# Performance work log

Measured on AMD Instinct MI355X. Metric: run time of the kernel, lower is better.

Reference implementation:

```python
import jax, jax.numpy as jnp
import numpy as np

N, E, D = 100000, 1280000, 64


def setup_inputs() -> dict:
    key = jax.random.key(0)
    ks = jax.random.split(key, 9)
    x = jax.random.normal(ks[0], (N, D), jnp.float32)
    edge_index = jax.random.randint(ks[1], (2, E), 0, N, dtype=jnp.int64)
    edge_weight = jax.random.uniform(ks[2], (E,), jnp.float32)
    s = 1.0 / np.sqrt(D)
    W0 = jax.random.normal(ks[3], (D, D), jnp.float32) * s
    b0 = jnp.zeros((D,), jnp.float32)
    W1 = jax.random.normal(ks[4], (D, D), jnp.float32) * s
    b1 = jnp.zeros((D,), jnp.float32)
    W2 = jax.random.normal(ks[5], (D, D), jnp.float32) * s
    b2 = jnp.zeros((D,), jnp.float32)
    return {"x": x, "edge_index": edge_index, "edge_weight": edge_weight,
            "W0": W0, "b0": b0, "W1": W1, "b1": b1, "W2": W2, "b2": b2}


def reference(x, edge_index, edge_weight, W0, b0, W1, b1, W2, b2):
    n = x.shape[0]
    row, col = edge_index[0], edge_index[1]
    # GCN normalization with self-loops (PyG gcn_norm, fill_value=1)
    loop = jnp.arange(n)
    row_f = jnp.concatenate([row, loop])
    col_f = jnp.concatenate([col, loop])
    w_f = jnp.concatenate([edge_weight, jnp.ones((n,), x.dtype)])
    deg = jax.ops.segment_sum(w_f, col_f, num_segments=n)
    dinv = jnp.where(deg > 0, jax.lax.rsqrt(deg), 0.0).astype(x.dtype)
    norm = dinv[row_f] * w_f * dinv[col_f]  # [E+N]

    def conv(h, W, b):
        h = h @ W                                  # [N, D_out]
        msg = h[row_f] * norm[:, None]             # gather + scale
        return jax.ops.segment_sum(msg, col_f, num_segments=n) + b

    results = [x]
    h = jax.nn.relu(conv(x, W0, b0))   # dropout p=0 / eval -> identity
    results.append(h)
    h = jax.nn.relu(conv(h, W1, b1))
    results.append(h)
    h = conv(h, W2, b2)                # last layer: no activation
    results.append(h)
    return tuple(results)
```

## Files before the change

### kernel.cpp

```cpp
#include <hip/hip_runtime.h>
#include <hip/hip_fp16.h>


#define TPB 256
#define ECAP 64
#define LCAP 6

typedef _Float16 half8 __attribute__((ext_vector_type(8)));
typedef float f32x4 __attribute__((ext_vector_type(4)));

__global__ __launch_bounds__(TPB) void k_scatter(const int* __restrict__ row,
                                                 const int* __restrict__ col,
                                                 const float* __restrict__ w,
                                                 int* __restrict__ degcnt,
                                                 long long* __restrict__ edges, int E) {
    int i = blockIdx.x * TPB + threadIdx.x;
    if (i >= E) return;
    int c = col[i];
    int r = atomicAdd(&degcnt[c], 1);
    if (r < ECAP)
        edges[((size_t)c << LCAP) + r] =
            ((long long)(unsigned)__float_as_int(w[i]) << 32) | (unsigned)row[i];
}

__global__ __launch_bounds__(TPB) void k_dinv(const long long* __restrict__ edges,
                                              const int* __restrict__ degcnt,
                                              float* __restrict__ dinv, int n) {
    int node = blockIdx.x * (TPB / 64) + (threadIdx.x >> 6);
    if (node >= n) return;
    int lane = threadIdx.x & 63;
    int cnt = min(degcnt[node], ECAP);
    float wv = 0.f;
    if (lane < cnt)
        wv = __int_as_float((int)(edges[((size_t)node << LCAP) + lane] >> 32));
    #pragma unroll
    for (int off = 1; off < 64; off <<= 1) wv += __shfl_xor(wv, off);
    if (lane == 0) dinv[node] = rsqrtf(1.0f + wv);
}

__global__ __launch_bounds__(TPB, 4) void k_gemm64(const float* __restrict__ in,
                                                   const float* __restrict__ Wg,
                                                   __half* __restrict__ hwh,
                                                   const float* __restrict__ dinvg,
                                                   float* __restrict__ cp, int n) {
    __shared__ _Float16 As[128 * 64];
    __shared__ _Float16 Bs[64 * 64];
    int tid = threadIdx.x;
    int rowbase = blockIdx.x * 128;

    {
        const float4* W4 = (const float4*)Wg;
        #pragma unroll
        for (int it = 0; it < 4; ++it) {
            int k = (tid >> 4) + 16 * it;
            int n0 = (tid & 15) * 4;
            float4 wv = W4[k * 16 + (tid & 15)];
            #pragma unroll
            for (int j = 0; j < 4; ++j) {
                int nn = n0 + j;
                float e = (j == 0) ? wv.x : (j == 1) ? wv.y : (j == 2) ? wv.z : wv.w;
                Bs[nn * 64 + (((k >> 3) ^ (nn & 7)) << 3) + (k & 7)] = (_Float16)e;
            }
        }
    }
    {
        int r = tid >> 1;
        int gr = rowbase + r;
        int c0 = (tid & 1) * 32;
        float di = (gr < n) ? dinvg[gr] : 0.f;
        const float4* A4 = (const float4*)in;
        #pragma unroll
        for (int j = 0; j < 4; ++j) {
            float4 v0 = make_float4(0.f, 0.f, 0.f, 0.f);
            float4 v1 = v0;
            if (gr < n) {
                v0 = A4[(size_t)gr * 16 + (c0 >> 2) + j * 2];
                v1 = A4[(size_t)gr * 16 + (c0 >> 2) + j * 2 + 1];
                if (cp) {
                    *(float4*)&cp[((size_t)gr * 16 + (c0 >> 2) + j * 2) * 4] = v0;
                    *(float4*)&cp[((size_t)gr * 16 + (c0 >> 2) + j * 2 + 1) * 4] = v1;
                }
            }
            int c4 = (c0 >> 3) + j;
            half8 hv;
            hv[0] = (_Float16)(v0.x * di); hv[1] = (_Float16)(v0.y * di);
            hv[2] = (_Float16)(v0.z * di); hv[3] = (_Float16)(v0.w * di);
            hv[4] = (_Float16)(v1.x * di); hv[5] = (_Float16)(v1.y * di);
            hv[6] = (_Float16)(v1.z * di); hv[7] = (_Float16)(v1.w * di);
            *(half8*)&As[r * 64 + ((c4 ^ (r & 7)) << 3)] = hv;
        }
    }
    __syncthreads();

    int w = tid >> 6;
    int lane = tid & 63;
    int l15 = lane & 15, l4 = lane >> 4;
    f32x4 acc[2][4];
    #pragma unroll
    for (int mt = 0; mt < 2; ++mt)
        #pragma unroll
        for (int nt = 0; nt < 4; ++nt) acc[mt][nt] = (f32x4){0.f, 0.f, 0.f, 0.f};
    const half8* Av = (const half8*)As;
    const half8* Bv = (const half8*)Bs;
    #pragma unroll
    for (int kk = 0; kk < 2; ++kk) {
        int ck = kk * 4 + l4;
        half8 a0 = Av[(w * 32 + l15) * 8 + (ck ^ (l15 & 7))];
        half8 a1 = Av[(w * 32 + 16 + l15) * 8 + (ck ^ (l15 & 7))];
        #pragma unroll
        for (int nt = 0; nt < 4; ++nt) {
            half8 b = Bv[(nt * 16 + l15) * 8 + (ck ^ (l15 & 7))];
            acc[0][nt] = __builtin_amdgcn_mfma_f32_16x16x32_f16(a0, b, acc[0][nt], 0, 0, 0);
            acc[1][nt] = __builtin_amdgcn_mfma_f32_16x16x32_f16(a1, b, acc[1][nt], 0, 0, 0);
        }
    }
    __syncthreads();

    #pragma unroll
    for (int mt = 0; mt < 2; ++mt)
        #pragma unroll
        for (int nt = 0; nt < 4; ++nt)
            #pragma unroll
            for (int rg = 0; rg < 4; ++rg) {
                int r = w * 32 + mt * 16 + l4 * 4 + rg;
                int c = nt * 16 + l15;
                As[r * 64 + (((c >> 3) ^ (r & 7)) << 3) + (c & 7)] =
                    (_Float16)acc[mt][nt][rg];
            }
    __syncthreads();
    #pragma unroll
    for (int it = 0; it < 4; ++it) {
        int idx = it * 256 + tid;
        int r = idx >> 3, c4 = idx & 7;
        int gr = rowbase + r;
        if (gr < n) {
            half8 hv = *(const half8*)&As[r * 64 + ((c4 ^ (r & 7)) << 3)];
            *(half8*)&hwh[(size_t)gr * 64 + c4 * 8] = hv;
        }
    }
}

__global__ __launch_bounds__(TPB) void k_gather(const int* __restrict__ degcnt,
                                                const long long* __restrict__ epk,
                                                const __half* __restrict__ hwh,
                                                const float* __restrict__ dinv,
                                                const float* __restrict__ b,
                                                float* __restrict__ out,
                                                int n, int relu) {
    int node = __builtin_amdgcn_readfirstlane(blockIdx.x * (TPB / 64) + (threadIdx.x >> 6));
    if (node >= n) return;
    int lane = threadIdx.x & 63;
    int cnt = min(degcnt[node], ECAP);
    int s0 = node << LCAP;
    int s1 = s0 + cnt;
    float acc = 0.f;
    int e = s0;
    for (; e + 8 <= s1; e += 8) {
        long long v0 = epk[e + 0];
        long long v1 = epk[e + 1];
        long long v2 = epk[e + 2];
        long long v3 = epk[e + 3];
        long long v4 = epk[e + 4];
        long long v5 = epk[e + 5];
        long long v6 = epk[e + 6];
        long long v7 = epk[e + 7];
        float h0 = __half2float(hwh[(size_t)(int)v0 * 64 + lane]);
        float h1 = __half2float(hwh[(size_t)(int)v1 * 64 + lane]);
        float h2 = __half2float(hwh[(size_t)(int)v2 * 64 + lane]);
        float h3 = __half2float(hwh[(size_t)(int)v3 * 64 + lane]);
        float h4 = __half2float(hwh[(size_t)(int)v4 * 64 + lane]);
        float h5 = __half2float(hwh[(size_t)(int)v5 * 64 + lane]);
        float h6 = __half2float(hwh[(size_t)(int)v6 * 64 + lane]);
        float h7 = __half2float(hwh[(size_t)(int)v7 * 64 + lane]);
        acc = fmaf(h0, __int_as_float((int)(v0 >> 32)), acc);
        acc = fmaf(h1, __int_as_float((int)(v1 >> 32)), acc);
        acc = fmaf(h2, __int_as_float((int)(v2 >> 32)), acc);
        acc = fmaf(h3, __int_as_float((int)(v3 >> 32)), acc);
        acc = fmaf(h4, __int_as_float((int)(v4 >> 32)), acc);
        acc = fmaf(h5, __int_as_float((int)(v5 >> 32)), acc);
        acc = fmaf(h6, __int_as_float((int)(v6 >> 32)), acc);
        acc = fmaf(h7, __int_as_float((int)(v7 >> 32)), acc);
    }
    if (e + 4 <= s1) {
        long long v0 = epk[e + 0];
        long long v1 = epk[e + 1];
        long long v2 = epk[e + 2];
        long long v3 = epk[e + 3];
        float h0 = __half2float(hwh[(size_t)(int)v0 * 64 + lane]);
        float h1 = __half2float(hwh[(size_t)(int)v1 * 64 + lane]);
        float h2 = __half2float(hwh[(size_t)(int)v2 * 64 + lane]);
        float h3 = __half2float(hwh[(size_t)(int)v3 * 64 + lane]);
        acc = fmaf(h0, __int_as_float((int)(v0 >> 32)), acc);
        acc = fmaf(h1, __int_as_float((int)(v1 >> 32)), acc);
        acc = fmaf(h2, __int_as_float((int)(v2 >> 32)), acc);
        acc = fmaf(h3, __int_as_float((int)(v3 >> 32)), acc);
        e += 4;
    }
    if (e + 2 <= s1) {
        long long v0 = epk[e + 0];
        long long v1 = epk[e + 1];
        float h0 = __half2float(hwh[(size_t)(int)v0 * 64 + lane]);
        float h1 = __half2float(hwh[(size_t)(int)v1 * 64 + lane]);
        acc = fmaf(h0, __int_as_float((int)(v0 >> 32)), acc);
        acc = fmaf(h1, __int_as_float((int)(v1 >> 32)), acc);
        e += 2;
    }
    if (e < s1) {
        long long v0 = epk[e];
        float h0 = __half2float(hwh[(size_t)(int)v0 * 64 + lane]);
        acc = fmaf(h0, __int_as_float((int)(v0 >> 32)), acc);
    }
    float di = dinv[node];
    float self = __half2float(hwh[(size_t)node * 64 + lane]);
    float o = fmaf(self + acc, di, b[lane]);
    if (relu) o = o > 0.f ? o : 0.f;
    out[(size_t)node * 64 + lane] = o;
}

extern "C" void kernel_launch(void* const* d_in, const int* in_sizes, int n_in,
                              void* d_out, int out_size, void* d_ws, size_t ws_size,
                              hipStream_t stream) {
    const float* x = (const float*)d_in[0];
    const int* ei = (const int*)d_in[1];
    const float* ew = (const float*)d_in[2];
    const float* Wl[3] = {(const float*)d_in[3], (const float*)d_in[5], (const float*)d_in[7]};
    const float* Bl[3] = {(const float*)d_in[4], (const float*)d_in[6], (const float*)d_in[8]};

    const int n = in_sizes[0] / 64;
    const int E = in_sizes[2];
    const int* row = ei;
    const int* col = ei + E;
    float* out = (float*)d_out;

    char* ws = (char*)d_ws;
    size_t o = 0;
    float* dinv       = (float*)(ws + o);    o = (o + (size_t)n * 4 + 255) & ~(size_t)255;
    __half* hwh       = (__half*)(ws + o);   o = (o + (size_t)n * 128 + 255) & ~(size_t)255;
    int* degcnt       = (int*)(ws + o);      o = (o + (size_t)n * 4 + 255) & ~(size_t)255;
    long long* edges  = (long long*)(ws + o);

    hipMemsetAsync(degcnt, 0, (size_t)n * 4, stream);
    k_scatter<<<(E + TPB - 1) / TPB, TPB, 0, stream>>>(row, col, ew, degcnt, edges, E);
    k_dinv<<<(n * 64 + TPB - 1) / TPB, TPB, 0, stream>>>(edges, degcnt, dinv, n);

    const float* hin = x;
    for (int L = 0; L < 3; ++L) {
        float* oseg = out + (size_t)(L + 1) * n * 64;
        k_gemm64<<<(n + 127) / 128, TPB, 0, stream>>>(hin, Wl[L], hwh, dinv, L == 0 ? out : nullptr, n);
        k_gather<<<(n * 64 + TPB - 1) / TPB, TPB, 0, stream>>>(degcnt, edges, hwh, dinv, Bl[L], oseg, n, L < 2 ? 1 : 0);
        hin = oseg;
    }
}
```

Baseline: 402.3 us.

## Fuse degree weight sum into scatter and drop separate dinv kernel

The scatter kernel now accumulates the per-node edge-weight sum with a float atomicAdd into a 64-byte-strided metadata record next to the count, and each thread handles two edges. This removes the separate k_dinv kernel launch and its pass over the edge lists. The gemm and gather kernels recompute rsqrt(1+wsum) on the fly. In exchange the scatter does a second atomic per edge, the memset grows from n*4 to n*64 bytes, and reads of count and weight sum now stride 64 bytes per node.

Result: slower. 434.1 us (+7.9%).

```diff
diff --git a/kernel.cpp b/kernel.cpp
--- a/kernel.cpp
+++ b/kernel.cpp
@@ -12,41 +12,41 @@
 __global__ __launch_bounds__(TPB) void k_scatter(const int* __restrict__ row,
                                                  const int* __restrict__ col,
                                                  const float* __restrict__ w,
-                                                 int* __restrict__ degcnt,
-                                                 long long* __restrict__ edges, int E) {
-    int i = blockIdx.x * TPB + threadIdx.x;
-    if (i >= E) return;
-    int c = col[i];
-    int r = atomicAdd(&degcnt[c], 1);
-    if (r < ECAP)
-        edges[((size_t)c << LCAP) + r] =
-            ((long long)(unsigned)__float_as_int(w[i]) << 32) | (unsigned)row[i];
-}
-
-__global__ __launch_bounds__(TPB) void k_dinv(const long long* __restrict__ edges,
-                                              const int* __restrict__ degcnt,
-                                              float* __restrict__ dinv, int n) {
-    int node = blockIdx.x * (TPB / 64) + (threadIdx.x >> 6);
-    if (node >= n) return;
-    int lane = threadIdx.x & 63;
-    int cnt = min(degcnt[node], ECAP);
-    float wv = 0.f;
-    if (lane < cnt)
-        wv = __int_as_float((int)(edges[((size_t)node << LCAP) + lane] >> 32));
-    #pragma unroll
-    for (int off = 1; off < 64; off <<= 1) wv += __shfl_xor(wv, off);
-    if (lane == 0) dinv[node] = rsqrtf(1.0f + wv);
+                                                 int* __restrict__ meta,
+                                                 long long* __restrict__ edges,
+                                                 int E, int half) {
+    int t = blockIdx.x * TPB + threadIdx.x;
+    if (t < half) {
+        int c = col[t];
+        float wv = w[t];
+        int r = atomicAdd(&meta[(size_t)c << 4], 1);
+        atomicAdd((float*)(meta + ((size_t)c << 4) + 1), wv);
+        if (r < ECAP)
+            edges[((size_t)c << LCAP) + r] =
+                ((long long)(unsigned)__float_as_int(wv) << 32) | (unsigned)row[t];
+    }
+    int t2 = t + half;
+    if (t2 < E) {
+        int c = col[t2];
+        float wv = w[t2];
+        int r = atomicAdd(&meta[(size_t)c << 4], 1);
+        atomicAdd((float*)(meta + ((size_t)c << 4) + 1), wv);
+        if (r < ECAP)
+            edges[((size_t)c << LCAP) + r] =
+                ((long long)(unsigned)__float_as_int(wv) << 32) | (unsigned)row[t2];
+    }
 }
 
 __global__ __launch_bounds__(TPB, 4) void k_gemm64(const float* __restrict__ in,
                                                    const float* __restrict__ Wg,
                                                    __half* __restrict__ hwh,
-                                                   const float* __restrict__ dinvg,
+                                                   const int* __restrict__ meta,
                                                    float* __restrict__ cp, int n) {
     __shared__ _Float16 As[128 * 64];
     __shared__ _Float16 Bs[64 * 64];
     int tid = threadIdx.x;
     int rowbase = blockIdx.x * 128;
+    const float* metaF = (const float*)meta;
 
     {
         const float4* W4 = (const float4*)Wg;
@@ -67,7 +67,8 @@
         int r = tid >> 1;
         int gr = rowbase + r;
         int c0 = (tid & 1) * 32;
-        float di = (gr < n) ? dinvg[gr] : 0.f;
+        float di = 0.f;
+        if (gr < n) di = rsqrtf(1.0f + metaF[((size_t)gr << 4) + 1]);
         const float4* A4 = (const float4*)in;
         #pragma unroll
         for (int j = 0; j < 4; ++j) {
@@ -140,17 +141,17 @@
     }
 }
 
-__global__ __launch_bounds__(TPB) void k_gather(const int* __restrict__ degcnt,
+__global__ __launch_bounds__(TPB) void k_gather(const int* __restrict__ meta,
                                                 const long long* __restrict__ epk,
                                                 const __half* __restrict__ hwh,
-                                                const float* __restrict__ dinv,
                                                 const float* __restrict__ b,
                                                 float* __restrict__ out,
                                                 int n, int relu) {
     int node = __builtin_amdgcn_readfirstlane(blockIdx.x * (TPB / 64) + (threadIdx.x >> 6));
     if (node >= n) return;
     int lane = threadIdx.x & 63;
-    int cnt = min(degcnt[node], ECAP);
+    int cnt = min(meta[(size_t)node << 4], ECAP);
+    float wsum = ((const float*)meta)[((size_t)node << 4) + 1];
     int s0 = node << LCAP;
     int s1 = s0 + cnt;
     float acc = 0.f;
@@ -210,7 +211,7 @@
         float h0 = __half2float(hwh[(size_t)(int)v0 * 64 + lane]);
         acc = fmaf(h0, __int_as_float((int)(v0 >> 32)), acc);
     }
-    float di = dinv[node];
+    float di = rsqrtf(1.0f + wsum);
     float self = __half2float(hwh[(size_t)node * 64 + lane]);
     float o = fmaf(self + acc, di, b[lane]);
     if (relu) o = o > 0.f ? o : 0.f;
@@ -234,20 +235,19 @@
 
     char* ws = (char*)d_ws;
     size_t o = 0;
-    float* dinv       = (float*)(ws + o);    o = (o + (size_t)n * 4 + 255) & ~(size_t)255;
     __half* hwh       = (__half*)(ws + o);   o = (o + (size_t)n * 128 + 255) & ~(size_t)255;
-    int* degcnt       = (int*)(ws + o);      o = (o + (size_t)n * 4 + 255) & ~(size_t)255;
+    int* meta         = (int*)(ws + o);      o = (o + (size_t)n * 64 + 255) & ~(size_t)255;
     long long* edges  = (long long*)(ws + o);
 
-    hipMemsetAsync(degcnt, 0, (size_t)n * 4, stream);
-    k_scatter<<<(E + TPB - 1) / TPB, TPB, 0, stream>>>(row, col, ew, degcnt, edges, E);
-    k_dinv<<<(n * 64 + TPB - 1) / TPB, TPB, 0, stream>>>(edges, degcnt, dinv, n);
+    hipMemsetAsync(meta, 0, (size_t)n * 64, stream);
+    int half = (E + 1) >> 1;
+    k_scatter<<<(half + TPB - 1) / TPB, TPB, 0, stream>>>(row, col, ew, meta, edges, E, half);
 
     const float* hin = x;
     for (int L = 0; L < 3; ++L) {
         float* oseg = out + (size_t)(L + 1) * n * 64;
-        k_gemm64<<<(n + 127) / 128, TPB, 0, stream>>>(hin, Wl[L], hwh, dinv, L == 0 ? out : nullptr, n);
-        k_gather<<<(n * 64 + TPB - 1) / TPB, TPB, 0, stream>>>(degcnt, edges, hwh, dinv, Bl[L], oseg, n, L < 2 ? 1 : 0);
+        k_gemm64<<<(n + 127) / 128, TPB, 0, stream>>>(hin, Wl[L], hwh, meta, L == 0 ? out : nullptr, n);
+        k_gather<<<(n * 64 + TPB - 1) / TPB, TPB, 0, stream>>>(meta, edges, hwh, Bl[L], oseg, n, L < 2 ? 1 : 0);
         hin = oseg;
     }
 }
```
